# Kernel tuning notes

Measured on AMD Instinct MI355X. Metric: run time of the kernel, lower is better.

The kernel has to match this reference:

```python
import jax, jax.numpy as jnp
import numpy as np

ALPHA = 1.5
TEMPERATURE = 1.0
N_ITER = 25
N_EMBED = 2048
NUM_EXPERTS = 64
N_TOKENS = 32768


def entmax_bisect(X, alpha=ALPHA, n_iter=N_ITER):
    """Faithful port of entmax.entmax_bisect forward (dim=-1)."""
    d = X.shape[-1]
    inv = 1.0 / (alpha - 1.0)
    Xa = X * (alpha - 1.0)
    max_val = jnp.max(Xa, axis=-1, keepdims=True)
    # _gp(1, alpha) = 1 ; _gp(1/d, alpha) = (1/d)**(1/(alpha-1))
    tau_lo = max_val - 1.0
    tau_hi = max_val - (1.0 / d) ** inv

    def p(tau):
        return jnp.clip(Xa - tau, 0.0, None) ** inv

    f_lo = jnp.sum(p(tau_lo), axis=-1, keepdims=True) - 1.0
    dm0 = tau_hi - tau_lo

    def body(carry, _):
        tau_lo, dm = carry
        dm = dm * 0.5
        tau_m = tau_lo + dm
        p_m = p(tau_m)
        f_m = jnp.sum(p_m, axis=-1, keepdims=True) - 1.0
        mask = (f_m * f_lo) >= 0
        tau_lo = jnp.where(mask, tau_m, tau_lo)
        return (tau_lo, dm), tau_m

    (tau_lo, dm), tau_ms = jax.lax.scan(body, (tau_lo, dm0), None, length=n_iter)
    tau_m_last = tau_ms[-1]  # [..., 1] tau used for the returned p_m in torch loop
    p_m = p(tau_m_last)
    # ensure_sum_one
    p_m = p_m / jnp.sum(p_m, axis=-1, keepdims=True)
    return p_m


def setup_inputs() -> dict:
    key = jax.random.key(0)
    kx, kw, kb = jax.random.split(key, 3)
    x = jax.random.normal(kx, (N_TOKENS, N_EMBED), dtype=jnp.float32)
    # nn.Linear default init: U(-1/sqrt(fan_in), 1/sqrt(fan_in))
    bound = 1.0 / np.sqrt(N_EMBED)
    W = jax.random.uniform(kw, (NUM_EXPERTS, N_EMBED), dtype=jnp.float32, minval=-bound, maxval=bound)
    b = jax.random.uniform(kb, (NUM_EXPERTS,), dtype=jnp.float32, minval=-bound, maxval=bound)
    return {"x": x, "W": W, "b": b}


def reference(x, W, b):
    logits = jnp.einsum("td,ed->te", x, W) + b  # [T, E]
    scaled_logits = logits / TEMPERATURE
    return entmax_bisect(scaled_logits)
```

## Files before the change

kernel.cpp:

```cpp
#include <hip/hip_runtime.h>
#include <hip/hip_bf16.h>
#include <stdint.h>

typedef _Float16 half8 __attribute__((ext_vector_type(8)));
typedef float    f32x4 __attribute__((ext_vector_type(4)));

#define N_EMBED   2048
#define N_EXP     64
#define KCHUNK    64
#define NKC       (N_EMBED / KCHUNK)
#define GCH       16
#define TILEB     8192
#define LGT_STRIDE 68
#define LGT_FLOATS (64 * LGT_STRIDE)

__global__ __launch_bounds__(64) void convert_w_kernel(
        const float* __restrict__ W, uint8_t* __restrict__ wsimg) {
    int tid = blockIdx.x * 64 + threadIdx.x;
    int e   = tid >> 8;
    int d0  = (tid & 255) * 8;
    int kc  = d0 >> 6;
    int dd0 = d0 & 63;
    const float* src = W + e * N_EMBED + d0;
    float4 f0 = *(const float4*)(src);
    float4 f1 = *(const float4*)(src + 4);
    float v[8] = {f0.x, f0.y, f0.z, f0.w, f1.x, f1.y, f1.z, f1.w};
    union { _Float16 h[8]; uint4 u; } hv;
#pragma unroll
    for (int j = 0; j < 8; ++j) hv.h[j] = (_Float16)(0.5f * v[j]);
    uint32_t off = (uint32_t)((e * 128 + dd0 * 2) ^ ((e & 7) << 4));
    *(uint4*)(wsimg + (size_t)kc * TILEB + off) = hv.u;
}

__device__ __forceinline__ half8 cvt8(f32x4 p, f32x4 q) {
    half8 h;
    h[0] = (_Float16)p[0]; h[1] = (_Float16)p[1];
    h[2] = (_Float16)p[2]; h[3] = (_Float16)p[3];
    h[4] = (_Float16)q[0]; h[5] = (_Float16)q[1];
    h[6] = (_Float16)q[2]; h[7] = (_Float16)q[3];
    return h;
}

__global__ __launch_bounds__(512, 4) void router_kernel(
        const float* __restrict__ x, const uint8_t* __restrict__ img,
        const float* __restrict__ bias, float* __restrict__ out) {
    __shared__ uint8_t lds[65536];

    const int tid  = threadIdx.x;
    const int wave = tid >> 6;
    const int lane = tid & 63;
    const int l15  = lane & 15;
    const int l4   = lane >> 4;
    const int g    = wave >> 2;
    const int q    = wave & 3;
    const int rowbase = blockIdx.x * 64;
    const float* xrow = x + (size_t)(rowbase + q * 16 + l15) * N_EMBED
                          + g * (GCH * KCHUNK) + l4 * 8;
    uint8_t* gring = lds + g * (4 * TILEB);

    uint32_t boff[4][2];
#pragma unroll
    for (int t = 0; t < 4; ++t)
#pragma unroll
        for (int s = 0; s < 2; ++s)
            boff[t][s] = (uint32_t)(((16 * t + l15) * 128 + s * 64 + l4 * 16)
                                    ^ ((l15 & 7) << 4));

    f32x4 acc[4];
#pragma unroll
    for (int t = 0; t < 4; ++t) acc[t] = (f32x4){0.f, 0.f, 0.f, 0.f};

    const int tg  = tid >> 8;
    const int t8  = tid & 255;
    auto STAGE2 = [&](int p) {
#pragma unroll
        for (int c = 0; c < 2; ++c) {
            int kc = 2 * p + c;
            const uint8_t* gsrc = img + (size_t)(tg * GCH + kc) * TILEB;
            uint8_t* dst = lds + tg * (4 * TILEB) + (kc & 3) * TILEB;
            __builtin_amdgcn_global_load_lds(
                (const __attribute__((address_space(1))) void*)(gsrc + t8 * 16),
                (__attribute__((address_space(3))) void*)(dst + t8 * 16),
                16, 0, 0);
            __builtin_amdgcn_global_load_lds(
                (const __attribute__((address_space(1))) void*)(gsrc + 4096 + t8 * 16),
                (__attribute__((address_space(3))) void*)(dst + 4096 + t8 * 16),
                16, 0, 0);
        }
    };

    f32x4 A0, A1, A2, A3, A4, A5, A6, A7;
    auto LOADA2 = [&](int p) {
        const float* ap = xrow + 2 * p * KCHUNK;
        A0 = __builtin_nontemporal_load((const f32x4*)(ap));
        A1 = __builtin_nontemporal_load((const f32x4*)(ap + 4));
        A2 = __builtin_nontemporal_load((const f32x4*)(ap + 32));
        A3 = __builtin_nontemporal_load((const f32x4*)(ap + 36));
        A4 = __builtin_nontemporal_load((const f32x4*)(ap + 64));
        A5 = __builtin_nontemporal_load((const f32x4*)(ap + 68));
        A6 = __builtin_nontemporal_load((const f32x4*)(ap + 96));
        A7 = __builtin_nontemporal_load((const f32x4*)(ap + 100));
    };
    auto MFMAS2 = [&](int p, half8 a0, half8 a1, half8 a2, half8 a3) {
        const uint8_t* lb0 = gring + (size_t)((2 * p) & 3) * TILEB;
        const uint8_t* lb1 = gring + (size_t)((2 * p + 1) & 3) * TILEB;
#pragma unroll
        for (int t = 0; t < 4; ++t) {
            half8 bh = *(const half8*)(lb0 + boff[t][0]);
            acc[t] = __builtin_amdgcn_mfma_f32_16x16x32_f16(a0, bh, acc[t], 0, 0, 0);
        }
#pragma unroll
        for (int t = 0; t < 4; ++t) {
            half8 bh = *(const half8*)(lb0 + boff[t][1]);
            acc[t] = __builtin_amdgcn_mfma_f32_16x16x32_f16(a1, bh, acc[t], 0, 0, 0);
        }
#pragma unroll
        for (int t = 0; t < 4; ++t) {
            half8 bh = *(const half8*)(lb1 + boff[t][0]);
            acc[t] = __builtin_amdgcn_mfma_f32_16x16x32_f16(a2, bh, acc[t], 0, 0, 0);
        }
#pragma unroll
        for (int t = 0; t < 4; ++t) {
            half8 bh = *(const half8*)(lb1 + boff[t][1]);
            acc[t] = __builtin_amdgcn_mfma_f32_16x16x32_f16(a3, bh, acc[t], 0, 0, 0);
        }
    };

    STAGE2(0);
    __builtin_amdgcn_sched_barrier(0);
    LOADA2(0);
    __builtin_amdgcn_sched_barrier(0);
    asm volatile("s_waitcnt vmcnt(8)" ::: "memory");
    __builtin_amdgcn_s_barrier();
    __builtin_amdgcn_sched_barrier(0);

#pragma unroll 1
    for (int p = 0; p < 7; ++p) {
        STAGE2(p + 1);
        __builtin_amdgcn_sched_barrier(0);
        {
            half8 a0 = cvt8(A0, A1);
            half8 a1 = cvt8(A2, A3);
            half8 a2 = cvt8(A4, A5);
            half8 a3 = cvt8(A6, A7);
            LOADA2(p + 1);
            MFMAS2(p, a0, a1, a2, a3);
        }
        asm volatile("s_waitcnt vmcnt(8) lgkmcnt(0)" ::: "memory");
        __builtin_amdgcn_s_barrier();
        __builtin_amdgcn_sched_barrier(0);
    }

    {
        half8 a0 = cvt8(A0, A1);
        half8 a1 = cvt8(A2, A3);
        half8 a2 = cvt8(A4, A5);
        half8 a3 = cvt8(A6, A7);
        MFMAS2(7, a0, a1, a2, a3);
    }

    __syncthreads();
    {
        float* lgt = (float*)lds + g * LGT_FLOATS;
#pragma unroll
        for (int t = 0; t < 4; ++t)
#pragma unroll
            for (int r = 0; r < 4; ++r)
                lgt[(q * 16 + l4 * 4 + r) * LGT_STRIDE + t * 16 + l15] = acc[t][r];
    }
    __syncthreads();

    const float* L0 = (const float*)lds;
    const float* L1 = L0 + LGT_FLOATS;
    const int row_local = wave * 8 + (lane >> 3);
    const int eb = (lane & 7) * 8;
    const int base = row_local * LGT_STRIDE + eb;

    float v0, v1, v2, v3, v4, v5, v6, v7;
    {
        float4 u0 = *(const float4*)(L0 + base);
        float4 u1 = *(const float4*)(L0 + base + 4);
        float4 w0 = *(const float4*)(L1 + base);
        float4 w1 = *(const float4*)(L1 + base + 4);
        float4 c0 = *(const float4*)(bias + eb);
        float4 c1 = *(const float4*)(bias + eb + 4);
        v0 = u0.x + w0.x + 0.5f * c0.x;
        v1 = u0.y + w0.y + 0.5f * c0.y;
        v2 = u0.z + w0.z + 0.5f * c0.z;
        v3 = u0.w + w0.w + 0.5f * c0.w;
        v4 = u1.x + w1.x + 0.5f * c1.x;
        v5 = u1.y + w1.y + 0.5f * c1.y;
        v6 = u1.z + w1.z + 0.5f * c1.z;
        v7 = u1.w + w1.w + 0.5f * c1.w;
    }

    float m = fmaxf(fmaxf(fmaxf(v0, v1), fmaxf(v2, v3)),
                    fmaxf(fmaxf(v4, v5), fmaxf(v6, v7)));
    m = fmaxf(m, __shfl_xor(m, 1, 64));
    m = fmaxf(m, __shfl_xor(m, 2, 64));
    m = fmaxf(m, __shfl_xor(m, 4, 64));

    float tau_lo = m - 1.0f;
    float tau_hi = m - 0.000244140625f;
    float dm = tau_hi - tau_lo;

    float s0;
    {
        float d;
        d = fmaxf(v0 - tau_lo, 0.f); s0 = d * d;
        d = fmaxf(v1 - tau_lo, 0.f); s0 = fmaf(d, d, s0);
        d = fmaxf(v2 - tau_lo, 0.f); s0 = fmaf(d, d, s0);
        d = fmaxf(v3 - tau_lo, 0.f); s0 = fmaf(d, d, s0);
        d = fmaxf(v4 - tau_lo, 0.f); s0 = fmaf(d, d, s0);
        d = fmaxf(v5 - tau_lo, 0.f); s0 = fmaf(d, d, s0);
        d = fmaxf(v6 - tau_lo, 0.f); s0 = fmaf(d, d, s0);
        d = fmaxf(v7 - tau_lo, 0.f); s0 = fmaf(d, d, s0);
    }
    s0 += __shfl_xor(s0, 1, 64);
    s0 += __shfl_xor(s0, 2, 64);
    s0 += __shfl_xor(s0, 4, 64);
    const float f_lo = s0 - 1.0f;

    float tau_m = tau_lo, fsum = 1.0f;
#pragma unroll 1
    for (int it = 0; it < 25; ++it) {
        dm *= 0.5f;
        tau_m = tau_lo + dm;
        float s, d;
        d = fmaxf(v0 - tau_m, 0.f); s = d * d;
        d = fmaxf(v1 - tau_m, 0.f); s = fmaf(d, d, s);
        d = fmaxf(v2 - tau_m, 0.f); s = fmaf(d, d, s);
        d = fmaxf(v3 - tau_m, 0.f); s = fmaf(d, d, s);
        d = fmaxf(v4 - tau_m, 0.f); s = fmaf(d, d, s);
        d = fmaxf(v5 - tau_m, 0.f); s = fmaf(d, d, s);
        d = fmaxf(v6 - tau_m, 0.f); s = fmaf(d, d, s);
        d = fmaxf(v7 - tau_m, 0.f); s = fmaf(d, d, s);
        s += __shfl_xor(s, 1, 64);
        s += __shfl_xor(s, 2, 64);
        s += __shfl_xor(s, 4, 64);
        if ((s - 1.0f) * f_lo >= 0.0f) tau_lo = tau_m;
        fsum = s;
    }
    float rinv = 1.0f / fsum;
    float4 o0, o1;
    {
        float d;
        d = fmaxf(v0 - tau_m, 0.f); o0.x = d * d * rinv;
        d = fmaxf(v1 - tau_m, 0.f); o0.y = d * d * rinv;
        d = fmaxf(v2 - tau_m, 0.f); o0.z = d * d * rinv;
        d = fmaxf(v3 - tau_m, 0.f); o0.w = d * d * rinv;
        d = fmaxf(v4 - tau_m, 0.f); o1.x = d * d * rinv;
        d = fmaxf(v5 - tau_m, 0.f); o1.y = d * d * rinv;
        d = fmaxf(v6 - tau_m, 0.f); o1.z = d * d * rinv;
        d = fmaxf(v7 - tau_m, 0.f); o1.w = d * d * rinv;
    }
    float* op = out + (size_t)(rowbase + row_local) * N_EXP + eb;
    *(float4*)(op)     = o0;
    *(float4*)(op + 4) = o1;
}

extern "C" void kernel_launch(void* const* d_in, const int* in_sizes, int n_in,
                              void* d_out, int out_size, void* d_ws, size_t ws_size,
                              hipStream_t stream) {
    (void)n_in; (void)out_size; (void)ws_size;
    const float* x  = (const float*)d_in[0];
    const float* W  = (const float*)d_in[1];
    const float* b  = (const float*)d_in[2];
    float* out      = (float*)d_out;
    uint8_t* wsimg  = (uint8_t*)d_ws;

    const int T = in_sizes[0] / N_EMBED;

    convert_w_kernel<<<dim3(256), dim3(64), 0, stream>>>(W, wsimg);
    router_kernel<<<dim3(T / 64), dim3(512), 0, stream>>>(x, wsimg, b, out);
}
```

Measured before the change: 73.32 us.

## Drop split-K across wave groups; each block handles 128 rows over full K

Before, two wave groups each covered half of K for 64 rows and combined partial logits through LDS. Now all 8 waves each own 16 rows across the full K, so a block covers 128 rows and runs 16 pipeline steps. The block stages a single shared W ring, which halves LDS use and halves the W traffic per row, and the entmax epilogue loops twice over 64 rows. The x loads also drop the nontemporal hint. The cost is half as many blocks (256), which may leave CUs less filled on a GPU with many CUs.

```diff
diff --git a/kernel.cpp b/kernel.cpp
--- a/kernel.cpp
+++ b/kernel.cpp
@@ -9,10 +9,8 @@
 #define N_EXP     64
 #define KCHUNK    64
 #define NKC       (N_EMBED / KCHUNK)
-#define GCH       16
 #define TILEB     8192
 #define LGT_STRIDE 68
-#define LGT_FLOATS (64 * LGT_STRIDE)
 
 __global__ __launch_bounds__(64) void convert_w_kernel(
         const float* __restrict__ W, uint8_t* __restrict__ wsimg) {
@@ -44,19 +42,16 @@
 __global__ __launch_bounds__(512, 4) void router_kernel(
         const float* __restrict__ x, const uint8_t* __restrict__ img,
         const float* __restrict__ bias, float* __restrict__ out) {
-    __shared__ uint8_t lds[65536];
+    __shared__ uint8_t lds[36864];
 
     const int tid  = threadIdx.x;
     const int wave = tid >> 6;
     const int lane = tid & 63;
     const int l15  = lane & 15;
     const int l4   = lane >> 4;
-    const int g    = wave >> 2;
-    const int q    = wave & 3;
-    const int rowbase = blockIdx.x * 64;
-    const float* xrow = x + (size_t)(rowbase + q * 16 + l15) * N_EMBED
-                          + g * (GCH * KCHUNK) + l4 * 8;
-    uint8_t* gring = lds + g * (4 * TILEB);
+    const int q    = wave;
+    const int rowbase = blockIdx.x * 128;
+    const float* xrow = x + (size_t)(rowbase + q * 16 + l15) * N_EMBED + l4 * 8;
 
     uint32_t boff[4][2];
 #pragma unroll
@@ -70,21 +65,16 @@
 #pragma unroll
     for (int t = 0; t < 4; ++t) acc[t] = (f32x4){0.f, 0.f, 0.f, 0.f};
 
-    const int tg  = tid >> 8;
-    const int t8  = tid & 255;
+    const int t9 = tid & 511;
     auto STAGE2 = [&](int p) {
 #pragma unroll
         for (int c = 0; c < 2; ++c) {
             int kc = 2 * p + c;
-            const uint8_t* gsrc = img + (size_t)(tg * GCH + kc) * TILEB;
-            uint8_t* dst = lds + tg * (4 * TILEB) + (kc & 3) * TILEB;
+            const uint8_t* gsrc = img + (size_t)kc * TILEB + t9 * 16;
+            uint8_t* dst = lds + (size_t)(kc & 3) * TILEB + t9 * 16;
             __builtin_amdgcn_global_load_lds(
-                (const __attribute__((address_space(1))) void*)(gsrc + t8 * 16),
-                (__attribute__((address_space(3))) void*)(dst + t8 * 16),
-                16, 0, 0);
-            __builtin_amdgcn_global_load_lds(
-                (const __attribute__((address_space(1))) void*)(gsrc + 4096 + t8 * 16),
-                (__attribute__((address_space(3))) void*)(dst + 4096 + t8 * 16),
+                (const __attribute__((address_space(1))) void*)gsrc,
+                (__attribute__((address_space(3))) void*)dst,
                 16, 0, 0);
         }
     };
@@ -92,18 +82,18 @@
     f32x4 A0, A1, A2, A3, A4, A5, A6, A7;
     auto LOADA2 = [&](int p) {
         const float* ap = xrow + 2 * p * KCHUNK;
-        A0 = __builtin_nontemporal_load((const f32x4*)(ap));
-        A1 = __builtin_nontemporal_load((const f32x4*)(ap + 4));
-        A2 = __builtin_nontemporal_load((const f32x4*)(ap + 32));
-        A3 = __builtin_nontemporal_load((const f32x4*)(ap + 36));
-        A4 = __builtin_nontemporal_load((const f32x4*)(ap + 64));
-        A5 = __builtin_nontemporal_load((const f32x4*)(ap + 68));
-        A6 = __builtin_nontemporal_load((const f32x4*)(ap + 96));
-        A7 = __builtin_nontemporal_load((const f32x4*)(ap + 100));
+        A0 = *(const f32x4*)(ap);
+        A1 = *(const f32x4*)(ap + 4);
+        A2 = *(const f32x4*)(ap + 32);
+        A3 = *(const f32x4*)(ap + 36);
+        A4 = *(const f32x4*)(ap + 64);
+        A5 = *(const f32x4*)(ap + 68);
+        A6 = *(const f32x4*)(ap + 96);
+        A7 = *(const f32x4*)(ap + 100);
     };
     auto MFMAS2 = [&](int p, half8 a0, half8 a1, half8 a2, half8 a3) {
-        const uint8_t* lb0 = gring + (size_t)((2 * p) & 3) * TILEB;
-        const uint8_t* lb1 = gring + (size_t)((2 * p + 1) & 3) * TILEB;
+        const uint8_t* lb0 = lds + (size_t)((2 * p) & 3) * TILEB;
+        const uint8_t* lb1 = lds + (size_t)((2 * p + 1) & 3) * TILEB;
 #pragma unroll
         for (int t = 0; t < 4; ++t) {
             half8 bh = *(const half8*)(lb0 + boff[t][0]);
@@ -135,7 +125,7 @@
     __builtin_amdgcn_sched_barrier(0);
 
 #pragma unroll 1
-    for (int p = 0; p < 7; ++p) {
+    for (int p = 0; p < 15; ++p) {
         STAGE2(p + 1);
         __builtin_amdgcn_sched_barrier(0);
         {
@@ -156,12 +146,12 @@
         half8 a1 = cvt8(A2, A3);
         half8 a2 = cvt8(A4, A5);
         half8 a3 = cvt8(A6, A7);
-        MFMAS2(7, a0, a1, a2, a3);
+        MFMAS2(15, a0, a1, a2, a3);
     }
 
     __syncthreads();
     {
-        float* lgt = (float*)lds + g * LGT_FLOATS;
+        float* lgt = (float*)lds;
 #pragma unroll
         for (int t = 0; t < 4; ++t)
 #pragma unroll
@@ -171,42 +161,40 @@
     __syncthreads();
 
     const float* L0 = (const float*)lds;
-    const float* L1 = L0 + LGT_FLOATS;
-    const int row_local = wave * 8 + (lane >> 3);
-    const int eb = (lane & 7) * 8;
-    const int base = row_local * LGT_STRIDE + eb;
-
-    float v0, v1, v2, v3, v4, v5, v6, v7;
-    {
-        float4 u0 = *(const float4*)(L0 + base);
-        float4 u1 = *(const float4*)(L0 + base + 4);
-        float4 w0 = *(const float4*)(L1 + base);
-        float4 w1 = *(const float4*)(L1 + base + 4);
-        float4 c0 = *(const float4*)(bias + eb);
-        float4 c1 = *(const float4*)(bias + eb + 4);
-        v0 = u0.x + w0.x + 0.5f * c0.x;
-        v1 = u0.y + w0.y + 0.5f * c0.y;
-        v2 = u0.z + w0.z + 0.5f * c0.z;
-        v3 = u0.w + w0.w + 0.5f * c0.w;
-        v4 = u1.x + w1.x + 0.5f * c1.x;
-        v5 = u1.y + w1.y + 0.5f * c1.y;
-        v6 = u1.z + w1.z + 0.5f * c1.z;
-        v7 = u1.w + w1.w + 0.5f * c1.w;
-    }
-
-    float m = fmaxf(fmaxf(fmaxf(v0, v1), fmaxf(v2, v3)),
-                    fmaxf(fmaxf(v4, v5), fmaxf(v6, v7)));
-    m = fmaxf(m, __shfl_xor(m, 1, 64));
-    m = fmaxf(m, __shfl_xor(m, 2, 64));
-    m = fmaxf(m, __shfl_xor(m, 4, 64));
-
-    float tau_lo = m - 1.0f;
-    float tau_hi = m - 0.000244140625f;
-    float dm = tau_hi - tau_lo;
-
-    float s0;
-    {
-        float d;
+    const int eb = (tid & 7) * 8;
+    float4 c0 = *(const float4*)(bias + eb);
+    float4 c1 = *(const float4*)(bias + eb + 4);
+
+#pragma unroll 1
+    for (int h = 0; h < 2; ++h) {
+        const int row_local = h * 64 + (tid >> 3);
+        const int base = row_local * LGT_STRIDE + eb;
+
+        float v0, v1, v2, v3, v4, v5, v6, v7;
+        {
+            float4 u0 = *(const float4*)(L0 + base);
+            float4 u1 = *(const float4*)(L0 + base + 4);
+            v0 = u0.x + 0.5f * c0.x;
+            v1 = u0.y + 0.5f * c0.y;
+            v2 = u0.z + 0.5f * c0.z;
+            v3 = u0.w + 0.5f * c0.w;
+            v4 = u1.x + 0.5f * c1.x;
+            v5 = u1.y + 0.5f * c1.y;
+            v6 = u1.z + 0.5f * c1.z;
+            v7 = u1.w + 0.5f * c1.w;
+        }
+
+        float m = fmaxf(fmaxf(fmaxf(v0, v1), fmaxf(v2, v3)),
+                        fmaxf(fmaxf(v4, v5), fmaxf(v6, v7)));
+        m = fmaxf(m, __shfl_xor(m, 1, 64));
+        m = fmaxf(m, __shfl_xor(m, 2, 64));
+        m = fmaxf(m, __shfl_xor(m, 4, 64));
+
+        float tau_lo = m - 1.0f;
+        float tau_hi = m - 0.000244140625f;
+        float dm = tau_hi - tau_lo;
+
+        float s0, d;
         d = fmaxf(v0 - tau_lo, 0.f); s0 = d * d;
         d = fmaxf(v1 - tau_lo, 0.f); s0 = fmaf(d, d, s0);
         d = fmaxf(v2 - tau_lo, 0.f); s0 = fmaf(d, d, s0);
@@ -215,36 +203,33 @@
         d = fmaxf(v5 - tau_lo, 0.f); s0 = fmaf(d, d, s0);
         d = fmaxf(v6 - tau_lo, 0.f); s0 = fmaf(d, d, s0);
         d = fmaxf(v7 - tau_lo, 0.f); s0 = fmaf(d, d, s0);
-    }
-    s0 += __shfl_xor(s0, 1, 64);
-    s0 += __shfl_xor(s0, 2, 64);
-    s0 += __shfl_xor(s0, 4, 64);
-    const float f_lo = s0 - 1.0f;
-
-    float tau_m = tau_lo, fsum = 1.0f;
+        s0 += __shfl_xor(s0, 1, 64);
+        s0 += __shfl_xor(s0, 2, 64);
+        s0 += __shfl_xor(s0, 4, 64);
+        const float f_lo = s0 - 1.0f;
+
+        float tau_m = tau_lo, fsum = 1.0f;
 #pragma unroll 1
-    for (int it = 0; it < 25; ++it) {
-        dm *= 0.5f;
-        tau_m = tau_lo + dm;
-        float s, d;
-        d = fmaxf(v0 - tau_m, 0.f); s = d * d;
-        d = fmaxf(v1 - tau_m, 0.f); s = fmaf(d, d, s);
-        d = fmaxf(v2 - tau_m, 0.f); s = fmaf(d, d, s);
-        d = fmaxf(v3 - tau_m, 0.f); s = fmaf(d, d, s);
-        d = fmaxf(v4 - tau_m, 0.f); s = fmaf(d, d, s);
-        d = fmaxf(v5 - tau_m, 0.f); s = fmaf(d, d, s);
-        d = fmaxf(v6 - tau_m, 0.f); s = fmaf(d, d, s);
-        d = fmaxf(v7 - tau_m, 0.f); s = fmaf(d, d, s);
-        s += __shfl_xor(s, 1, 64);
-        s += __shfl_xor(s, 2, 64);
-        s += __shfl_xor(s, 4, 64);
-        if ((s - 1.0f) * f_lo >= 0.0f) tau_lo = tau_m;
-        fsum = s;
-    }
-    float rinv = 1.0f / fsum;
-    float4 o0, o1;
-    {
-        float d;
+        for (int it = 0; it < 25; ++it) {
+            dm *= 0.5f;
+            tau_m = tau_lo + dm;
+            float s;
+            d = fmaxf(v0 - tau_m, 0.f); s = d * d;
+            d = fmaxf(v1 - tau_m, 0.f); s = fmaf(d, d, s);
+            d = fmaxf(v2 - tau_m, 0.f); s = fmaf(d, d, s);
+            d = fmaxf(v3 - tau_m, 0.f); s = fmaf(d, d, s);
+            d = fmaxf(v4 - tau_m, 0.f); s = fmaf(d, d, s);
+            d = fmaxf(v5 - tau_m, 0.f); s = fmaf(d, d, s);
+            d = fmaxf(v6 - tau_m, 0.f); s = fmaf(d, d, s);
+            d = fmaxf(v7 - tau_m, 0.f); s = fmaf(d, d, s);
+            s += __shfl_xor(s, 1, 64);
+            s += __shfl_xor(s, 2, 64);
+            s += __shfl_xor(s, 4, 64);
+            if ((s - 1.0f) * f_lo >= 0.0f) tau_lo = tau_m;
+            fsum = s;
+        }
+        float rinv = 1.0f / fsum;
+        float4 o0, o1;
         d = fmaxf(v0 - tau_m, 0.f); o0.x = d * d * rinv;
         d = fmaxf(v1 - tau_m, 0.f); o0.y = d * d * rinv;
         d = fmaxf(v2 - tau_m, 0.f); o0.z = d * d * rinv;
@@ -253,10 +238,11 @@
         d = fmaxf(v5 - tau_m, 0.f); o1.y = d * d * rinv;
         d = fmaxf(v6 - tau_m, 0.f); o1.z = d * d * rinv;
         d = fmaxf(v7 - tau_m, 0.f); o1.w = d * d * rinv;
-    }
-    float* op = out + (size_t)(rowbase + row_local) * N_EXP + eb;
-    *(float4*)(op)     = o0;
-    *(float4*)(op + 4) = o1;
+
+        float* op = out + (size_t)(rowbase + row_local) * N_EXP + eb;
+        *(float4*)(op)     = o0;
+        *(float4*)(op + 4) = o1;
+    }
 }
 
 extern "C" void kernel_launch(void* const* d_in, const int* in_sizes, int n_in,
@@ -272,5 +258,5 @@
     const int T = in_sizes[0] / N_EMBED;
 
     convert_w_kernel<<<dim3(256), dim3(64), 0, stream>>>(W, wsimg);
-    router_kernel<<<dim3(T / 64), dim3(512), 0, stream>>>(x, wsimg, b, out);
-}
+    router_kernel<<<dim3(T / 128), dim3(512), 0, stream>>>(x, wsimg, b, out);
+}
```

New measurement: 64.66 us. 11.8% less time.

## Shrink router blocks to 32 rows with single-chunk double-buffered pipeline

Applied to the files above, without the earlier changes.

Halves the block to 256 threads covering 32 tokens, cuts LDS from 64KB to 32KB, and replaces the 4-deep two-chunk ring with a two-slot single-chunk double buffer. The x loads change from nontemporal to ordinary loads, and the wait counts are adjusted to match. The aim is higher occupancy and more blocks to hide latency. The cost is that each W tile in LDS is reused across half as many rows, which doubles W traffic per token and the barrier count per K-chunk. A dead STAGE2 lambda remains in the code.

```diff
diff --git a/kernel.cpp b/kernel.cpp
--- a/kernel.cpp
+++ b/kernel.cpp
@@ -12,7 +12,7 @@
 #define GCH       16
 #define TILEB     8192
 #define LGT_STRIDE 68
-#define LGT_FLOATS (64 * LGT_STRIDE)
+#define LGT_FLOATS (32 * LGT_STRIDE)
 
 __global__ __launch_bounds__(64) void convert_w_kernel(
         const float* __restrict__ W, uint8_t* __restrict__ wsimg) {
@@ -41,22 +41,22 @@
     return h;
 }
 
-__global__ __launch_bounds__(512, 4) void router_kernel(
+__global__ __launch_bounds__(256, 4) void router_kernel(
         const float* __restrict__ x, const uint8_t* __restrict__ img,
         const float* __restrict__ bias, float* __restrict__ out) {
-    __shared__ uint8_t lds[65536];
+    __shared__ uint8_t lds[32768];
 
     const int tid  = threadIdx.x;
     const int wave = tid >> 6;
     const int lane = tid & 63;
     const int l15  = lane & 15;
     const int l4   = lane >> 4;
-    const int g    = wave >> 2;
-    const int q    = wave & 3;
-    const int rowbase = blockIdx.x * 64;
+    const int g    = wave >> 1;
+    const int q    = wave & 1;
+    const int rowbase = blockIdx.x * 32;
     const float* xrow = x + (size_t)(rowbase + q * 16 + l15) * N_EMBED
                           + g * (GCH * KCHUNK) + l4 * 8;
-    uint8_t* gring = lds + g * (4 * TILEB);
+    uint8_t* gbase = lds + g * 16384;
 
     uint32_t boff[4][2];
 #pragma unroll
@@ -70,83 +70,67 @@
 #pragma unroll
     for (int t = 0; t < 4; ++t) acc[t] = (f32x4){0.f, 0.f, 0.f, 0.f};
 
-    const int tg  = tid >> 8;
-    const int t8  = tid & 255;
+    const int tg = tid >> 7;
+    const int t7 = tid & 127;
     auto STAGE2 = [&](int p) {
-#pragma unroll
-        for (int c = 0; c < 2; ++c) {
-            int kc = 2 * p + c;
-            const uint8_t* gsrc = img + (size_t)(tg * GCH + kc) * TILEB;
-            uint8_t* dst = lds + tg * (4 * TILEB) + (kc & 3) * TILEB;
+        const uint8_t* gsrc = img + (size_t)(tg * GCH + 2 * p) * TILEB + t7 * 16;
+        uint8_t* dst = lds + tg * 16384 + (p & 1) * 8192 + t7 * 16;
+        (void)gsrc; (void)dst;
+    };
+    (void)STAGE2;
+    auto STAGE1 = [&](int kc) {
+        const uint8_t* gsrc = img + (size_t)(tg * GCH + kc) * TILEB;
+        uint8_t* dst = lds + tg * 16384 + (kc & 1) * 8192;
+#pragma unroll
+        for (int j = 0; j < 4; ++j) {
             __builtin_amdgcn_global_load_lds(
-                (const __attribute__((address_space(1))) void*)(gsrc + t8 * 16),
-                (__attribute__((address_space(3))) void*)(dst + t8 * 16),
+                (const __attribute__((address_space(1))) void*)(gsrc + j * 2048 + t7 * 16),
+                (__attribute__((address_space(3))) void*)(dst + j * 2048 + t7 * 16),
                 16, 0, 0);
-            __builtin_amdgcn_global_load_lds(
-                (const __attribute__((address_space(1))) void*)(gsrc + 4096 + t8 * 16),
-                (__attribute__((address_space(3))) void*)(dst + 4096 + t8 * 16),
-                16, 0, 0);
-        }
-    };
-
-    f32x4 A0, A1, A2, A3, A4, A5, A6, A7;
-    auto LOADA2 = [&](int p) {
-        const float* ap = xrow + 2 * p * KCHUNK;
-        A0 = __builtin_nontemporal_load((const f32x4*)(ap));
-        A1 = __builtin_nontemporal_load((const f32x4*)(ap + 4));
-        A2 = __builtin_nontemporal_load((const f32x4*)(ap + 32));
-        A3 = __builtin_nontemporal_load((const f32x4*)(ap + 36));
-        A4 = __builtin_nontemporal_load((const f32x4*)(ap + 64));
-        A5 = __builtin_nontemporal_load((const f32x4*)(ap + 68));
-        A6 = __builtin_nontemporal_load((const f32x4*)(ap + 96));
-        A7 = __builtin_nontemporal_load((const f32x4*)(ap + 100));
-    };
-    auto MFMAS2 = [&](int p, half8 a0, half8 a1, half8 a2, half8 a3) {
-        const uint8_t* lb0 = gring + (size_t)((2 * p) & 3) * TILEB;
-        const uint8_t* lb1 = gring + (size_t)((2 * p + 1) & 3) * TILEB;
+        }
+    };
+
+    f32x4 A0, A1, A2, A3;
+    auto LOADA1 = [&](int kc) {
+        const float* ap = xrow + kc * KCHUNK;
+        A0 = *(const f32x4*)(ap);
+        A1 = *(const f32x4*)(ap + 4);
+        A2 = *(const f32x4*)(ap + 32);
+        A3 = *(const f32x4*)(ap + 36);
+    };
+    auto MFMAS1 = [&](int kc, half8 a0, half8 a1) {
+        const uint8_t* lb = gbase + (size_t)(kc & 1) * 8192;
 #pragma unroll
         for (int t = 0; t < 4; ++t) {
-            half8 bh = *(const half8*)(lb0 + boff[t][0]);
+            half8 bh = *(const half8*)(lb + boff[t][0]);
             acc[t] = __builtin_amdgcn_mfma_f32_16x16x32_f16(a0, bh, acc[t], 0, 0, 0);
         }
 #pragma unroll
         for (int t = 0; t < 4; ++t) {
-            half8 bh = *(const half8*)(lb0 + boff[t][1]);
+            half8 bh = *(const half8*)(lb + boff[t][1]);
             acc[t] = __builtin_amdgcn_mfma_f32_16x16x32_f16(a1, bh, acc[t], 0, 0, 0);
         }
-#pragma unroll
-        for (int t = 0; t < 4; ++t) {
-            half8 bh = *(const half8*)(lb1 + boff[t][0]);
-            acc[t] = __builtin_amdgcn_mfma_f32_16x16x32_f16(a2, bh, acc[t], 0, 0, 0);
-        }
-#pragma unroll
-        for (int t = 0; t < 4; ++t) {
-            half8 bh = *(const half8*)(lb1 + boff[t][1]);
-            acc[t] = __builtin_amdgcn_mfma_f32_16x16x32_f16(a3, bh, acc[t], 0, 0, 0);
-        }
-    };
-
-    STAGE2(0);
+    };
+
+    STAGE1(0);
     __builtin_amdgcn_sched_barrier(0);
-    LOADA2(0);
+    LOADA1(0);
     __builtin_amdgcn_sched_barrier(0);
-    asm volatile("s_waitcnt vmcnt(8)" ::: "memory");
+    asm volatile("s_waitcnt vmcnt(4)" ::: "memory");
     __builtin_amdgcn_s_barrier();
     __builtin_amdgcn_sched_barrier(0);
 
 #pragma unroll 1
-    for (int p = 0; p < 7; ++p) {
-        STAGE2(p + 1);
+    for (int kc = 0; kc < GCH - 1; ++kc) {
+        STAGE1(kc + 1);
         __builtin_amdgcn_sched_barrier(0);
         {
             half8 a0 = cvt8(A0, A1);
             half8 a1 = cvt8(A2, A3);
-            half8 a2 = cvt8(A4, A5);
-            half8 a3 = cvt8(A6, A7);
-            LOADA2(p + 1);
-            MFMAS2(p, a0, a1, a2, a3);
-        }
-        asm volatile("s_waitcnt vmcnt(8) lgkmcnt(0)" ::: "memory");
+            LOADA1(kc + 1);
+            MFMAS1(kc, a0, a1);
+        }
+        asm volatile("s_waitcnt vmcnt(4) lgkmcnt(0)" ::: "memory");
         __builtin_amdgcn_s_barrier();
         __builtin_amdgcn_sched_barrier(0);
     }
@@ -154,9 +138,7 @@
     {
         half8 a0 = cvt8(A0, A1);
         half8 a1 = cvt8(A2, A3);
-        half8 a2 = cvt8(A4, A5);
-        half8 a3 = cvt8(A6, A7);
-        MFMAS2(7, a0, a1, a2, a3);
+        MFMAS1(GCH - 1, a0, a1);
     }
 
     __syncthreads();
@@ -172,8 +154,8 @@
 
     const float* L0 = (const float*)lds;
     const float* L1 = L0 + LGT_FLOATS;
-    const int row_local = wave * 8 + (lane >> 3);
-    const int eb = (lane & 7) * 8;
+    const int row_local = tid >> 3;
+    const int eb = (tid & 7) * 8;
     const int base = row_local * LGT_STRIDE + eb;
 
     float v0, v1, v2, v3, v4, v5, v6, v7;
@@ -204,18 +186,15 @@
     float tau_hi = m - 0.000244140625f;
     float dm = tau_hi - tau_lo;
 
-    float s0;
-    {
-        float d;
-        d = fmaxf(v0 - tau_lo, 0.f); s0 = d * d;
-        d = fmaxf(v1 - tau_lo, 0.f); s0 = fmaf(d, d, s0);
-        d = fmaxf(v2 - tau_lo, 0.f); s0 = fmaf(d, d, s0);
-        d = fmaxf(v3 - tau_lo, 0.f); s0 = fmaf(d, d, s0);
-        d = fmaxf(v4 - tau_lo, 0.f); s0 = fmaf(d, d, s0);
-        d = fmaxf(v5 - tau_lo, 0.f); s0 = fmaf(d, d, s0);
-        d = fmaxf(v6 - tau_lo, 0.f); s0 = fmaf(d, d, s0);
-        d = fmaxf(v7 - tau_lo, 0.f); s0 = fmaf(d, d, s0);
-    }
+    float s0, d;
+    d = fmaxf(v0 - tau_lo, 0.f); s0 = d * d;
+    d = fmaxf(v1 - tau_lo, 0.f); s0 = fmaf(d, d, s0);
+    d = fmaxf(v2 - tau_lo, 0.f); s0 = fmaf(d, d, s0);
+    d = fmaxf(v3 - tau_lo, 0.f); s0 = fmaf(d, d, s0);
+    d = fmaxf(v4 - tau_lo, 0.f); s0 = fmaf(d, d, s0);
+    d = fmaxf(v5 - tau_lo, 0.f); s0 = fmaf(d, d, s0);
+    d = fmaxf(v6 - tau_lo, 0.f); s0 = fmaf(d, d, s0);
+    d = fmaxf(v7 - tau_lo, 0.f); s0 = fmaf(d, d, s0);
     s0 += __shfl_xor(s0, 1, 64);
     s0 += __shfl_xor(s0, 2, 64);
     s0 += __shfl_xor(s0, 4, 64);
@@ -226,7 +205,7 @@
     for (int it = 0; it < 25; ++it) {
         dm *= 0.5f;
         tau_m = tau_lo + dm;
-        float s, d;
+        float s;
         d = fmaxf(v0 - tau_m, 0.f); s = d * d;
         d = fmaxf(v1 - tau_m, 0.f); s = fmaf(d, d, s);
         d = fmaxf(v2 - tau_m, 0.f); s = fmaf(d, d, s);
@@ -243,17 +222,15 @@
     }
     float rinv = 1.0f / fsum;
     float4 o0, o1;
-    {
-        float d;
-        d = fmaxf(v0 - tau_m, 0.f); o0.x = d * d * rinv;
-        d = fmaxf(v1 - tau_m, 0.f); o0.y = d * d * rinv;
-        d = fmaxf(v2 - tau_m, 0.f); o0.z = d * d * rinv;
-        d = fmaxf(v3 - tau_m, 0.f); o0.w = d * d * rinv;
-        d = fmaxf(v4 - tau_m, 0.f); o1.x = d * d * rinv;
-        d = fmaxf(v5 - tau_m, 0.f); o1.y = d * d * rinv;
-        d = fmaxf(v6 - tau_m, 0.f); o1.z = d * d * rinv;
-        d = fmaxf(v7 - tau_m, 0.f); o1.w = d * d * rinv;
-    }
+    d = fmaxf(v0 - tau_m, 0.f); o0.x = d * d * rinv;
+    d = fmaxf(v1 - tau_m, 0.f); o0.y = d * d * rinv;
+    d = fmaxf(v2 - tau_m, 0.f); o0.z = d * d * rinv;
+    d = fmaxf(v3 - tau_m, 0.f); o0.w = d * d * rinv;
+    d = fmaxf(v4 - tau_m, 0.f); o1.x = d * d * rinv;
+    d = fmaxf(v5 - tau_m, 0.f); o1.y = d * d * rinv;
+    d = fmaxf(v6 - tau_m, 0.f); o1.z = d * d * rinv;
+    d = fmaxf(v7 - tau_m, 0.f); o1.w = d * d * rinv;
+
     float* op = out + (size_t)(rowbase + row_local) * N_EXP + eb;
     *(float4*)(op)     = o0;
     *(float4*)(op + 4) = o1;
@@ -272,5 +249,5 @@
     const int T = in_sizes[0] / N_EMBED;
 
     convert_w_kernel<<<dim3(256), dim3(64), 0, stream>>>(W, wsimg);
-    router_kernel<<<dim3(T / 64), dim3(512), 0, stream>>>(x, wsimg, b, out);
-}
+    router_kernel<<<dim3(T / 32), dim3(256), 0, stream>>>(x, wsimg, b, out);
+}
```

Result: faster. 66.25 us (-9.6%).
